# Optimization experiments

Measured on AMD Instinct MI355X. Metric: run time of the kernel, lower is better.

The kernel has to match this reference:

```python
import jax, jax.numpy as jnp
import numpy as np

N = 100000
E = 3200000
HOP = 10

def setup_inputs() -> dict:
    key = jax.random.key(0)
    ks = jax.random.split(key, 10)
    n_in, n_hid, n_out = 512, 256, 64
    x = jax.random.normal(ks[0], (N, n_in), dtype=jnp.float32)
    edge_row = jax.random.randint(ks[1], (E,), 0, N, dtype=jnp.int32)
    edge_col = jax.random.randint(ks[2], (E,), 0, N, dtype=jnp.int32)
    # row-normalized-ish positive edge values (like a transition matrix)
    edge_vals = jax.random.uniform(ks[3], (E,), dtype=jnp.float32) / 32.0
    A2 = jax.random.uniform(ks[4], (N, 1), dtype=jnp.float32)
    # xavier-ish init scaled down for numerical sanity
    W1 = jax.random.normal(ks[5], (n_in, n_hid), dtype=jnp.float32) * (2.0 / (n_in + n_hid)) ** 0.5
    b1 = jnp.zeros((n_hid,), dtype=jnp.float32)
    W3 = jax.random.normal(ks[6], (n_hid, n_hid), dtype=jnp.float32) * (2.0 / (2 * n_hid)) ** 0.5
    b3 = jnp.zeros((n_hid,), dtype=jnp.float32)
    W2 = jax.random.normal(ks[7], (n_hid, n_out), dtype=jnp.float32) * (2.0 / (n_hid + n_out)) ** 0.5
    b2 = jnp.zeros((n_out,), dtype=jnp.float32)
    return {"x": x, "edge_row": edge_row, "edge_col": edge_col, "edge_vals": edge_vals,
            "A2": A2, "W1": W1, "b1": b1, "W3": W3, "b3": b3, "W2": W2, "b2": b2}

def _spmm(edge_row, edge_col, edge_vals, h):
    # sparse [N,N] @ dense [N,F] via gather + segment_sum
    msgs = edge_vals[:, None] * h[edge_col]          # [E, F]
    return jax.ops.segment_sum(msgs, edge_row, num_segments=N)

def reference(x, edge_row, edge_col, edge_vals, A2, W1, b1, W3, b3, W2, b2):
    # dropout layers are identity at eval time
    x0 = jax.nn.relu(x @ W1 + b1)                    # [N, n_hid]
    h = x0
    for _ in range(HOP):
        h = _spmm(edge_row, edge_col, edge_vals, h) + A2 * x0
        h = jax.nn.relu(h + h @ W3 + b3)
    return h @ W2 + b2                               # [N, n_out]
```

## Files before the change

kernel.cpp:

```cpp
#include <hip/hip_runtime.h>
#include <stdint.h>


typedef unsigned short bf16_t;
typedef __attribute__((ext_vector_type(8))) short bf16x8;
typedef __attribute__((ext_vector_type(4))) float f32x4;

__device__ __forceinline__ float bf2f(bf16_t u) {
    union { unsigned int i; float f; } v; v.i = ((unsigned int)u) << 16; return v.f;
}
__device__ __forceinline__ bf16_t f2bf(float f) {
    union { float f; unsigned int i; } v; v.f = f;
    unsigned int x = v.i;
    unsigned int r = (x + 0x7fffu + ((x >> 16) & 1u)) >> 16;
    return (bf16_t)r;
}

__global__ void zero_i32(int* __restrict__ p, int n) {
    int i = blockIdx.x * blockDim.x + threadIdx.x;
    if (i < n) p[i] = 0;
}

__global__ void transpose_w(const float* __restrict__ W, bf16_t* __restrict__ Wt,
                            int K, int N) {
    int i = blockIdx.x * blockDim.x + threadIdx.x;
    if (i < K * N) {
        int k = i / N, n = i % N;
        Wt[(size_t)n * K + k] = f2bf(W[i]);
    }
}

__global__ void count_edges(const int* __restrict__ er, const int* __restrict__ ec,
                            int* __restrict__ cnt, int E, int N) {
    int i = blockIdx.x * blockDim.x + threadIdx.x;
    if (i < E) {
        unsigned r = (unsigned)er[i], c = (unsigned)ec[i];
        if (r < (unsigned)N && c < (unsigned)N) atomicAdd(&cnt[r], 1);
    }
}

__global__ __launch_bounds__(1024)
void scan_rows(int* cnt_cursor, int* __restrict__ row_ptr, int n) {
    __shared__ int sums[1024];
    int t = threadIdx.x;
    int chunk = (n + 1023) >> 10;
    int start = t * chunk;
    int end = min(start + chunk, n);
    int s = 0;
    for (int i = start; i < end; ++i) s += cnt_cursor[i];
    sums[t] = s;
    __syncthreads();
    for (int off = 1; off < 1024; off <<= 1) {
        int v = (t >= off) ? sums[t - off] : 0;
        __syncthreads();
        sums[t] += v;
        __syncthreads();
    }
    int run = (t == 0) ? 0 : sums[t - 1];
    for (int i = start; i < end; ++i) {
        int c = cnt_cursor[i];
        row_ptr[i] = run;
        cnt_cursor[i] = run;
        run += c;
    }
    if (t == 1023) row_ptr[n] = sums[1023];
}

__global__ void scatter_edges(const int* __restrict__ er, const int* __restrict__ ec,
                              const float* __restrict__ ev, int* __restrict__ cursor,
                              int2* __restrict__ csr, int E, int N) {
    int i = blockIdx.x * blockDim.x + threadIdx.x;
    if (i < E) {
        unsigned r = (unsigned)er[i], c = (unsigned)ec[i];
        if (r < (unsigned)N && c < (unsigned)N) {
            int p = atomicAdd(&cursor[r], 1);
            csr[p] = make_int2((int)c, __float_as_int(ev[i]));
        }
    }
}

__global__ __launch_bounds__(256)
void spmm_kernel(const int* __restrict__ row_ptr, const int2* __restrict__ csr,
                 const bf16_t* __restrict__ h, const bf16_t* __restrict__ x0,
                 const float* __restrict__ A2, bf16_t* __restrict__ s, int N) {
    int w = threadIdx.x >> 6;
    int lane = threadIdx.x & 63;
    int row = (blockIdx.x << 2) + w;
    if (row >= N) return;
    int fo = lane << 2;
    int base = (row << 8) + fo;
    float a2 = A2[row];
    ushort4 xv = *(const ushort4*)&x0[base];
    float acc0 = a2 * bf2f(xv.x);
    float acc1 = a2 * bf2f(xv.y);
    float acc2 = a2 * bf2f(xv.z);
    float acc3 = a2 * bf2f(xv.w);
    int e = row_ptr[row], e1 = row_ptr[row + 1];
    for (; e + 4 <= e1; e += 4) {
        int2 p0 = csr[e], p1 = csr[e + 1], p2 = csr[e + 2], p3 = csr[e + 3];
        ushort4 h0 = *(const ushort4*)&h[(p0.x << 8) + fo];
        ushort4 h1 = *(const ushort4*)&h[(p1.x << 8) + fo];
        ushort4 h2 = *(const ushort4*)&h[(p2.x << 8) + fo];
        ushort4 h3 = *(const ushort4*)&h[(p3.x << 8) + fo];
        float v0 = __int_as_float(p0.y), v1 = __int_as_float(p1.y);
        float v2 = __int_as_float(p2.y), v3 = __int_as_float(p3.y);
        acc0 += v0 * bf2f(h0.x); acc1 += v0 * bf2f(h0.y);
        acc2 += v0 * bf2f(h0.z); acc3 += v0 * bf2f(h0.w);
        acc0 += v1 * bf2f(h1.x); acc1 += v1 * bf2f(h1.y);
        acc2 += v1 * bf2f(h1.z); acc3 += v1 * bf2f(h1.w);
        acc0 += v2 * bf2f(h2.x); acc1 += v2 * bf2f(h2.y);
        acc2 += v2 * bf2f(h2.z); acc3 += v2 * bf2f(h2.w);
        acc0 += v3 * bf2f(h3.x); acc1 += v3 * bf2f(h3.y);
        acc2 += v3 * bf2f(h3.z); acc3 += v3 * bf2f(h3.w);
    }
    for (; e < e1; ++e) {
        int2 p = csr[e];
        ushort4 hv = *(const ushort4*)&h[(p.x << 8) + fo];
        float v = __int_as_float(p.y);
        acc0 += v * bf2f(hv.x); acc1 += v * bf2f(hv.y);
        acc2 += v * bf2f(hv.z); acc3 += v * bf2f(hv.w);
    }
    ushort4 o;
    o.x = f2bf(acc0); o.y = f2bf(acc1); o.z = f2bf(acc2); o.w = f2bf(acc3);
    *(ushort4*)&s[base] = o;
}

template <int WM, int WN, bool AF32, bool SKIP, bool RELU, typename CT>
__global__ __launch_bounds__(256)
void mfma_gemm(const void* __restrict__ Av, const bf16_t* __restrict__ Bt,
               const float* __restrict__ bias, CT* __restrict__ C,
               int M, int K, int Nfull) {
    constexpr int TM = WM * 64;
    constexpr int TN = WN * 64;
    __shared__ bf16_t As[TM * 32];
    __shared__ bf16_t Bs[TN * 32];
    const int tid = threadIdx.x;
    const int w = tid >> 6, lane = tid & 63;
    const int q = lane >> 4, l16 = lane & 15;
    const int bm = blockIdx.x * TM;
    const int bn = blockIdx.y * TN;
    const int wm = (w % WM) * 64;
    const int wn = (w / WM) * 64;

    f32x4 acc[4][4] = {};

    for (int k0 = 0; k0 < K; k0 += 32) {
        if constexpr (AF32) {
            const float* A = (const float*)Av;
            int row = tid >> 1;
            int gr = min(bm + row, M - 1);
            const float* src = A + (size_t)gr * K + k0 + (tid & 1) * 16;
            bf16_t* dst = As + row * 32 + (tid & 1) * 16;
            #pragma unroll
            for (int g = 0; g < 4; ++g) {
                float4 v = *(const float4*)(src + 4 * g);
                ushort4 u;
                u.x = f2bf(v.x); u.y = f2bf(v.y); u.z = f2bf(v.z); u.w = f2bf(v.w);
                *(ushort4*)(dst + 4 * g) = u;
            }
        } else {
            const bf16_t* A = (const bf16_t*)Av;
            #pragma unroll
            for (int r = 0; r < TM / 64; ++r) {
                int rowbase = r * 64 + w * 16;
                int row = rowbase + (lane >> 2);
                int gr = min(bm + row, M - 1);
                const bf16_t* gp = A + (size_t)gr * K + k0 + (lane & 3) * 8;
                bf16_t* lp = As + rowbase * 32 + lane * 8;
                __builtin_amdgcn_global_load_lds(
                    (const __attribute__((address_space(1))) unsigned int*)gp,
                    (__attribute__((address_space(3))) unsigned int*)lp, 16, 0, 0);
            }
        }
        #pragma unroll
        for (int r = 0; r < TN / 64; ++r) {
            int rowbase = r * 64 + w * 16;
            int row = rowbase + (lane >> 2);
            const bf16_t* gp = Bt + (size_t)(bn + row) * K + k0 + (lane & 3) * 8;
            bf16_t* lp = Bs + rowbase * 32 + lane * 8;
            __builtin_amdgcn_global_load_lds(
                (const __attribute__((address_space(1))) unsigned int*)gp,
                (__attribute__((address_space(3))) unsigned int*)lp, 16, 0, 0);
        }
        __syncthreads();

        bf16x8 afr[4], bfr[4];
        #pragma unroll
        for (int ms = 0; ms < 4; ++ms)
            afr[ms] = *(const bf16x8*)&As[(wm + ms * 16 + l16) * 32 + q * 8];
        #pragma unroll
        for (int ns = 0; ns < 4; ++ns)
            bfr[ns] = *(const bf16x8*)&Bs[(wn + ns * 16 + l16) * 32 + q * 8];
        #pragma unroll
        for (int ms = 0; ms < 4; ++ms)
            #pragma unroll
            for (int ns = 0; ns < 4; ++ns)
                acc[ms][ns] = __builtin_amdgcn_mfma_f32_16x16x32_bf16(
                    afr[ms], bfr[ns], acc[ms][ns], 0, 0, 0);
        __syncthreads();
    }

    const bf16_t* Askip = (const bf16_t*)Av;
    #pragma unroll
    for (int ms = 0; ms < 4; ++ms) {
        #pragma unroll
        for (int r = 0; r < 4; ++r) {
            int row = bm + wm + ms * 16 + q * 4 + r;
            if (row < M) {
                #pragma unroll
                for (int ns = 0; ns < 4; ++ns) {
                    int col = bn + wn + ns * 16 + l16;
                    float v = acc[ms][ns][r] + bias[col];
                    if constexpr (SKIP) v += bf2f(Askip[(size_t)row * K + col]);
                    if constexpr (RELU) v = fmaxf(v, 0.f);
                    if constexpr (sizeof(CT) == 2) C[(size_t)row * Nfull + col] = (CT)f2bf(v);
                    else                           C[(size_t)row * Nfull + col] = (CT)v;
                }
            }
        }
    }
}

extern "C" void kernel_launch(void* const* d_in, const int* in_sizes, int n_in,
                              void* d_out, int out_size, void* d_ws, size_t ws_size,
                              hipStream_t stream) {
    const float* x   = (const float*)d_in[0];
    const int* erow  = (const int*)d_in[1];
    const int* ecol  = (const int*)d_in[2];
    const float* ev  = (const float*)d_in[3];
    const float* A2  = (const float*)d_in[4];
    const float* W1  = (const float*)d_in[5];
    const float* b1  = (const float*)d_in[6];
    const float* W3  = (const float*)d_in[7];
    const float* b3  = (const float*)d_in[8];
    const float* W2  = (const float*)d_in[9];
    const float* b2  = (const float*)d_in[10];
    float* out = (float*)d_out;

    const int N   = in_sizes[4];
    const int E   = in_sizes[1];
    const int NIN = in_sizes[0] / N;
    const int NH  = in_sizes[6];
    const int NO  = in_sizes[10];
    if (NH != 256 || NIN != 512 || NO != 64) return;

    char* ws = (char*)d_ws;
    size_t off = 0;
    auto alloc = [&](size_t bytes) -> void* {
        void* p = ws + off;
        off += (bytes + 255) & ~(size_t)255;
        return p;
    };
    bf16_t* x0     = (bf16_t*)alloc((size_t)N * NH * 2);
    bf16_t* hA     = (bf16_t*)alloc((size_t)N * NH * 2);
    bf16_t* hB     = (bf16_t*)alloc((size_t)N * NH * 2);
    int*   row_ptr = (int*)alloc((size_t)(N + 1) * 4);
    int*   cursor  = (int*)alloc((size_t)N * 4);
    int2*  csr     = (int2*)alloc((size_t)E * 8);
    bf16_t* W1t    = (bf16_t*)alloc((size_t)NIN * NH * 2);
    bf16_t* W3t    = (bf16_t*)alloc((size_t)NH * NH * 2);
    bf16_t* W2t    = (bf16_t*)alloc((size_t)NH * NO * 2);
    if (off > ws_size) return;

    zero_i32<<<(N + 255) / 256, 256, 0, stream>>>(cursor, N);
    count_edges<<<(E + 255) / 256, 256, 0, stream>>>(erow, ecol, cursor, E, N);
    scan_rows<<<1, 1024, 0, stream>>>(cursor, row_ptr, N);
    scatter_edges<<<(E + 255) / 256, 256, 0, stream>>>(erow, ecol, ev, cursor,
                                                       csr, E, N);
    transpose_w<<<(NIN * NH + 255) / 256, 256, 0, stream>>>(W1, W1t, NIN, NH);
    transpose_w<<<(NH * NH + 255) / 256, 256, 0, stream>>>(W3, W3t, NH, NH);
    transpose_w<<<(NH * NO + 255) / 256, 256, 0, stream>>>(W2, W2t, NH, NO);

    dim3 g1((N + 127) / 128, NH / 128);
    mfma_gemm<2, 2, true, false, true, bf16_t><<<g1, 256, 0, stream>>>(
        x, W1t, b1, x0, N, NIN, NH);

    const bf16_t* hin = x0;
    for (int hop = 0; hop < 10; ++hop) {
        spmm_kernel<<<(N + 3) / 4, 256, 0, stream>>>(row_ptr, csr, hin, x0, A2, hB, N);
        mfma_gemm<2, 2, false, true, true, bf16_t><<<g1, 256, 0, stream>>>(
            hB, W3t, b3, hA, N, NH, NH);
        hin = hA;
    }

    dim3 g2((N + 255) / 256, 1);
    mfma_gemm<4, 1, false, false, false, float><<<g2, 256, 0, stream>>>(
        hA, W2t, b2, out, N, NH, NO);
}
```

Before: 3.641 ms.

## Build CSR via two-level binning with shared-memory bucket sort

Replaces the per-edge global atomic scatter into CSR with a two-pass scheme. Edges are first binned into 256-row buckets using per-block shared-memory counts and one global atomic per bucket per block. Each bucket is then sorted by local row in shared memory. This cuts global atomic contention and random writes during CSR construction, at the cost of an extra pass over the edge array, row-local bits packed into the column field, and a bucket capacity limit that falls back to global reads when exceeded.

```diff
diff --git a/kernel.cpp b/kernel.cpp
--- a/kernel.cpp
+++ b/kernel.cpp
@@ -30,12 +30,12 @@
     }
 }
 
-__global__ void count_edges(const int* __restrict__ er, const int* __restrict__ ec,
-                            int* __restrict__ cnt, int E, int N) {
+__global__ void count_edges(const int* __restrict__ er, int* __restrict__ cnt,
+                            int E, int N) {
     int i = blockIdx.x * blockDim.x + threadIdx.x;
     if (i < E) {
-        unsigned r = (unsigned)er[i], c = (unsigned)ec[i];
-        if (r < (unsigned)N && c < (unsigned)N) atomicAdd(&cnt[r], 1);
+        unsigned r = (unsigned)er[i];
+        if (r < (unsigned)N) atomicAdd(&cnt[r], 1);
     }
 }
 
@@ -60,22 +60,90 @@
     for (int i = start; i < end; ++i) {
         int c = cnt_cursor[i];
         row_ptr[i] = run;
-        cnt_cursor[i] = run;
         run += c;
     }
     if (t == 1023) row_ptr[n] = sums[1023];
 }
 
-__global__ void scatter_edges(const int* __restrict__ er, const int* __restrict__ ec,
-                              const float* __restrict__ ev, int* __restrict__ cursor,
-                              int2* __restrict__ csr, int E, int N) {
-    int i = blockIdx.x * blockDim.x + threadIdx.x;
-    if (i < E) {
-        unsigned r = (unsigned)er[i], c = (unsigned)ec[i];
-        if (r < (unsigned)N && c < (unsigned)N) {
-            int p = atomicAdd(&cursor[r], 1);
-            csr[p] = make_int2((int)c, __float_as_int(ev[i]));
+__global__ void init_bcur(const int* __restrict__ row_ptr, int* __restrict__ bcur,
+                          int N, int NB) {
+    int b = blockIdx.x * blockDim.x + threadIdx.x;
+    if (b < NB) bcur[b] = row_ptr[min(b << 8, N)];
+}
+
+#define BIN_CHUNK 8192
+#define NBMAX 392
+__global__ __launch_bounds__(256)
+void bin_edges(const int* __restrict__ er, const int* __restrict__ ec,
+               const float* __restrict__ ev, int* __restrict__ bcur,
+               int2* __restrict__ binned, int E, int N, int NB) {
+    __shared__ int cnt[NBMAX];
+    __shared__ int resv[NBMAX];
+    int tid = threadIdx.x;
+    int e0 = blockIdx.x * BIN_CHUNK;
+    int n = min(BIN_CHUNK, E - e0);
+    for (int b = tid; b < NB; b += 256) cnt[b] = 0;
+    __syncthreads();
+    for (int i = tid; i < n; i += 256) {
+        unsigned r = (unsigned)er[e0 + i];
+        if (r < (unsigned)N) atomicAdd(&cnt[r >> 8], 1);
+    }
+    __syncthreads();
+    for (int b = tid; b < NB; b += 256) {
+        int c = cnt[b];
+        resv[b] = c ? atomicAdd(&bcur[b], c) : 0;
+        cnt[b] = 0;
+    }
+    __syncthreads();
+    for (int i = tid; i < n; i += 256) {
+        unsigned r = (unsigned)er[e0 + i];
+        if (r < (unsigned)N) {
+            unsigned c = (unsigned)ec[e0 + i];
+            float v = ev[e0 + i];
+            if (c >= (unsigned)N) { c = 0; v = 0.f; }
+            int b = (int)(r >> 8);
+            int p = resv[b] + atomicAdd(&cnt[b], 1);
+            binned[p] = make_int2((int)(((r & 255u) << 17) | c), __float_as_int(v));
         }
+    }
+}
+
+#define BCAP 9216
+__global__ __launch_bounds__(256)
+void bucket_sort(const int* __restrict__ row_ptr, int2* __restrict__ csr, int N) {
+    __shared__ int2 ent[BCAP];
+    __shared__ int cnt[256];
+    __shared__ int base[256];
+    __shared__ int lcur[256];
+    int b = blockIdx.x;
+    int tid = threadIdx.x;
+    int r0 = b << 8;
+    int e0 = row_ptr[r0];
+    int e1 = row_ptr[min(r0 + 256, N)];
+    int n = e1 - e0;
+    cnt[tid] = 0;
+    __syncthreads();
+    for (int i = tid; i < n; i += 256) {
+        int2 p = csr[e0 + i];
+        if (i < BCAP) ent[i] = p;
+        atomicAdd(&cnt[((unsigned)p.x >> 17) & 255u], 1);
+    }
+    __syncthreads();
+    int v0 = cnt[tid];
+    for (int off = 1; off < 256; off <<= 1) {
+        int u = (tid >= off) ? cnt[tid - off] : 0;
+        __syncthreads();
+        cnt[tid] += u;
+        __syncthreads();
+    }
+    base[tid] = cnt[tid] - v0;
+    lcur[tid] = 0;
+    __syncthreads();
+    for (int i = tid; i < n; i += 256) {
+        int2 p = (i < BCAP) ? ent[i] : csr[e0 + i];
+        int rl = (int)(((unsigned)p.x >> 17) & 255u);
+        int d = base[rl] + atomicAdd(&lcur[rl], 1);
+        csr[e0 + d] = make_int2(p.x & 0x1FFFF, p.y);
     }
 }
 
@@ -243,6 +311,8 @@
     const int NH  = in_sizes[6];
     const int NO  = in_sizes[10];
     if (NH != 256 || NIN != 512 || NO != 64) return;
+    const int NB = (N + 255) >> 8;
+    if (NB > NBMAX) return;
 
     char* ws = (char*)d_ws;
     size_t off = 0;
@@ -255,18 +325,21 @@
     bf16_t* hA     = (bf16_t*)alloc((size_t)N * NH * 2);
     bf16_t* hB     = (bf16_t*)alloc((size_t)N * NH * 2);
     int*   row_ptr = (int*)alloc((size_t)(N + 1) * 4);
-    int*   cursor  = (int*)alloc((size_t)N * 4);
+    int*   counts  = (int*)alloc((size_t)N * 4);
+    int*   bcur    = (int*)alloc((size_t)NB * 4);
     int2*  csr     = (int2*)alloc((size_t)E * 8);
     bf16_t* W1t    = (bf16_t*)alloc((size_t)NIN * NH * 2);
     bf16_t* W3t    = (bf16_t*)alloc((size_t)NH * NH * 2);
     bf16_t* W2t    = (bf16_t*)alloc((size_t)NH * NO * 2);
     if (off > ws_size) return;
 
-    zero_i32<<<(N + 255) / 256, 256, 0, stream>>>(cursor, N);
-    count_edges<<<(E + 255) / 256, 256, 0, stream>>>(erow, ecol, cursor, E, N);
-    scan_rows<<<1, 1024, 0, stream>>>(cursor, row_ptr, N);
-    scatter_edges<<<(E + 255) / 256, 256, 0, stream>>>(erow, ecol, ev, cursor,
-                                                       csr, E, N);
+    zero_i32<<<(N + 255) / 256, 256, 0, stream>>>(counts, N);
+    count_edges<<<(E + 255) / 256, 256, 0, stream>>>(erow, counts, E, N);
+    scan_rows<<<1, 1024, 0, stream>>>(counts, row_ptr, N);
+    init_bcur<<<(NB + 255) / 256, 256, 0, stream>>>(row_ptr, bcur, N, NB);
+    bin_edges<<<(E + BIN_CHUNK - 1) / BIN_CHUNK, 256, 0, stream>>>(
+        erow, ecol, ev, bcur, csr, E, N, NB);
+    bucket_sort<<<NB, 256, 0, stream>>>(row_ptr, csr, N);
     transpose_w<<<(NIN * NH + 255) / 256, 256, 0, stream>>>(W1, W1t, NIN, NH);
     transpose_w<<<(NH * NH + 255) / 256, 256, 0, stream>>>(W3, W3t, NH, NH);
     transpose_w<<<(NH * NO + 255) / 256, 256, 0, stream>>>(W2, W2t, NH, NO);
```

After: 3.439 ms. 5.5% less time.
